# Kernel tuning notes

Hardware: AMD Instinct MI355X
Metric: run time of the kernel (lower is better)

## Reference

```python
import jax, jax.numpy as jnp
import numpy as np

R = 8
INPUT_DIM = 2048
OUTPUT_DIM = 2048
SCALING = 16.0 / R  # lora_alpha / r
TEMPERATURE = 1.0
LN_EPS = 1e-5


def setup_inputs() -> dict:
    key = jax.random.key(0)
    ks = jax.random.split(key, 6)
    bs, seq, ctr_out, ctr_final = 8, 2048, 32, 4
    x = jax.random.normal(ks[0], (bs, seq, INPUT_DIM), dtype=jnp.float32)
    ctr = jax.random.normal(ks[1], (bs, ctr_out), dtype=jnp.float32)
    W1 = jax.random.normal(ks[2], (60, ctr_out), dtype=jnp.float32) * (1.0 / np.sqrt(ctr_out))
    b1 = jnp.zeros((60,), jnp.float32)
    W2 = jax.random.normal(ks[3], (ctr_final, 60), dtype=jnp.float32) * (1.0 / np.sqrt(60))
    b2 = jnp.zeros((ctr_final,), jnp.float32)
    Wa = jax.random.normal(ks[4], (INPUT_DIM * R, ctr_final), dtype=jnp.float32) * 0.02
    Wb = jax.random.normal(ks[5], (R * OUTPUT_DIM, ctr_final), dtype=jnp.float32) * 0.02
    return {
        'x': x, 'ctr_hidden_states': ctr,
        'ln_gamma': jnp.ones((ctr_out,), jnp.float32),
        'ln_beta': jnp.zeros((ctr_out,), jnp.float32),
        'W1': W1, 'b1': b1, 'W2': W2, 'b2': b2, 'Wa': Wa, 'Wb': Wb,
    }


def reference(x, ctr_hidden_states, ln_gamma, ln_beta, W1, b1, W2, b2, Wa, Wb):
    bs = x.shape[0]
    # gating MLP (default which_in_gate branch): LN -> Linear -> ReLU -> Linear
    mu = jnp.mean(ctr_hidden_states, axis=-1, keepdims=True)
    var = jnp.mean(jnp.square(ctr_hidden_states - mu), axis=-1, keepdims=True)
    z = (ctr_hidden_states - mu) * jax.lax.rsqrt(var + LN_EPS) * ln_gamma + ln_beta
    h = jax.nn.relu(z @ W1.T + b1)                 # [bs, 60]
    gate = h @ W2.T + b2                           # [bs, ctr_final_dim]
    # soft routing with softmax
    gate = jax.nn.softmax(gate / TEMPERATURE, axis=-1)
    # per-sample low-rank adapters
    A = (gate @ Wa.T).reshape(bs, R, INPUT_DIM)    # [bs, r, d_in]
    B = (gate @ Wb.T).reshape(bs, R, OUTPUT_DIM)   # [bs, r, d_out]
    # out = (x @ A^T) @ B * scaling
    xa = jnp.einsum('bsd,brd->bsr', x, A)          # [bs, seq, r]
    out = jnp.einsum('bsr,bro->bso', xa, B) * SCALING
    return out
```

## Files before the change

### kernel.cpp

```cpp
#include <hip/hip_runtime.h>
#include <math.h>


#define BS 8
#define SEQ 2048
#define DIM 2048
#define RR 8
#define SCALING 2.0f

typedef float vf4 __attribute__((ext_vector_type(4)));

__global__ void gate_ab_kernel(const float* __restrict__ ctr,
                               const float* __restrict__ gamma,
                               const float* __restrict__ beta,
                               const float* __restrict__ W1,
                               const float* __restrict__ b1,
                               const float* __restrict__ W2,
                               const float* __restrict__ b2,
                               const float* __restrict__ Wa,
                               const float* __restrict__ Wb,
                               float* __restrict__ A,
                               float* __restrict__ B) {
    __shared__ float z_s[BS][32];
    __shared__ float h_s[BS][60];
    __shared__ float logit_s[BS][4];
    __shared__ float gate_s[BS][4];
    const int tid = threadIdx.x;

    {
        const int b = tid >> 5, i = tid & 31;
        float v = ctr[b * 32 + i];
        float s = v;
        #pragma unroll
        for (int m = 16; m; m >>= 1) s += __shfl_xor(s, m, 64);
        const float mu = s * (1.0f / 32.0f);
        const float d = v - mu;
        float sq = d * d;
        #pragma unroll
        for (int m = 16; m; m >>= 1) sq += __shfl_xor(sq, m, 64);
        const float var = sq * (1.0f / 32.0f);
        z_s[b][i] = d * rsqrtf(var + 1e-5f) * gamma[i] + beta[i];
    }
    __syncthreads();

    for (int idx = tid; idx < BS * 60; idx += 256) {
        const int b = idx / 60, j = idx % 60;
        float acc = b1[j];
        #pragma unroll
        for (int k = 0; k < 32; ++k) acc += z_s[b][k] * W1[j * 32 + k];
        h_s[b][j] = fmaxf(acc, 0.0f);
    }
    __syncthreads();

    if (tid < 32) {
        const int b = tid >> 2, c = tid & 3;
        float acc = b2[c];
        for (int k = 0; k < 60; ++k) acc += h_s[b][k] * W2[c * 60 + k];
        logit_s[b][c] = acc;
    }
    __syncthreads();

    if (tid < 8) {
        float m = logit_s[tid][0];
        #pragma unroll
        for (int c = 1; c < 4; ++c) m = fmaxf(m, logit_s[tid][c]);
        float e[4], s = 0.0f;
        #pragma unroll
        for (int c = 0; c < 4; ++c) { e[c] = expf(logit_s[tid][c] - m); s += e[c]; }
        const float inv = 1.0f / s;
        #pragma unroll
        for (int c = 0; c < 4; ++c) gate_s[tid][c] = e[c] * inv;
    }
    __syncthreads();

    const vf4* __restrict__ Wa4 = (const vf4*)Wa;
    const vf4* __restrict__ Wb4 = (const vf4*)Wb;
    const int total = BS * RR * DIM;
    for (int idx = blockIdx.x * 256 + tid; idx < total; idx += gridDim.x * 256) {
        const int b = idx >> 14, rd = idx & 16383;
        const vf4 g = *(const vf4*)gate_s[b];
        const vf4 wa = Wa4[rd];
        A[idx] = g.x * wa.x + g.y * wa.y + g.z * wa.z + g.w * wa.w;
        const vf4 wb = Wb4[rd];
        B[idx] = SCALING * (g.x * wb.x + g.y * wb.y + g.z * wb.z + g.w * wb.w);
    }
}

__global__ void __launch_bounds__(256, 4)
xa_kernel(const float* __restrict__ x, const float* __restrict__ A,
          float* __restrict__ xa) {
    const int b    = blockIdx.x >> 7;
    const int tile = blockIdx.x & 127;
    const int wave = threadIdx.x >> 6, lane = threadIdx.x & 63;
    const int row0 = tile * 16 + wave * 4;

    const float* __restrict__ xr = x + ((size_t)(b * SEQ + row0)) * DIM;
    const float* __restrict__ Ab = A + b * (RR * DIM);

    float acc[4][8];
    #pragma unroll
    for (int i = 0; i < 4; ++i)
        #pragma unroll
        for (int r = 0; r < 8; ++r) acc[i][r] = 0.0f;

    vf4 xcur[4], xnxt[4];
    {
        const int d0 = lane * 4;
        #pragma unroll
        for (int i = 0; i < 4; ++i)
            xcur[i] = *(const vf4*)&xr[(size_t)i * DIM + d0];
    }
    #pragma unroll
    for (int j = 0; j < 8; ++j) {
        const int d = j * 256 + lane * 4;
        if (j < 7) {
            #pragma unroll
            for (int i = 0; i < 4; ++i)
                xnxt[i] = *(const vf4*)&xr[(size_t)i * DIM + d + 256];
        }
        vf4 a4[8];
        #pragma unroll
        for (int r = 0; r < 8; ++r) a4[r] = *(const vf4*)&Ab[r * DIM + d];
        #pragma unroll
        for (int i = 0; i < 4; ++i) {
            #pragma unroll
            for (int r = 0; r < 8; ++r)
                acc[i][r] += xcur[i].x * a4[r].x + xcur[i].y * a4[r].y +
                             xcur[i].z * a4[r].z + xcur[i].w * a4[r].w;
        }
        #pragma unroll
        for (int i = 0; i < 4; ++i) xcur[i] = xnxt[i];
    }

    float xv[4][8];
    #pragma unroll
    for (int i = 0; i < 4; ++i) {
        #pragma unroll
        for (int r = 0; r < 8; ++r) {
            float v = acc[i][r];
            #pragma unroll
            for (int off = 32; off; off >>= 1) v += __shfl_xor(v, off, 64);
            xv[i][r] = v;
        }
    }

    if (lane < 32) {
        float v = 0.0f;
        #pragma unroll
        for (int i = 0; i < 4; ++i)
            #pragma unroll
            for (int r = 0; r < 8; ++r)
                if (lane == i * 8 + r) v = xv[i][r];
        xa[((size_t)(b * SEQ + row0)) * RR + lane] = v;
    }
}

__global__ void __launch_bounds__(256, 4)
out_kernel(const float* __restrict__ xa, const float* __restrict__ B,
           float* __restrict__ out) {
    const int b    = blockIdx.x >> 7;
    const int tile = blockIdx.x & 127;
    const int wave = threadIdx.x >> 6, lane = threadIdx.x & 63;
    const int row0 = tile * 16 + wave * 4;

    const float* __restrict__ Bb = B + b * (RR * DIM);
    float* __restrict__ ob = out + ((size_t)(b * SEQ + row0)) * DIM;

    float xv[4][8];
    #pragma unroll
    for (int i = 0; i < 4; ++i) {
        const vf4 lo = *(const vf4*)&xa[((size_t)(b * SEQ + row0 + i)) * RR];
        const vf4 hi = *(const vf4*)&xa[((size_t)(b * SEQ + row0 + i)) * RR + 4];
        xv[i][0] = lo.x; xv[i][1] = lo.y; xv[i][2] = lo.z; xv[i][3] = lo.w;
        xv[i][4] = hi.x; xv[i][5] = hi.y; xv[i][6] = hi.z; xv[i][7] = hi.w;
    }

    #pragma unroll
    for (int j = 0; j < 8; ++j) {
        const int o = j * 256 + lane * 4;
        vf4 b4[8];
        #pragma unroll
        for (int r = 0; r < 8; ++r) b4[r] = *(const vf4*)&Bb[r * DIM + o];
        #pragma unroll
        for (int i = 0; i < 4; ++i) {
            vf4 v = {0.0f, 0.0f, 0.0f, 0.0f};
            #pragma unroll
            for (int r = 0; r < 8; ++r) {
                v.x += xv[i][r] * b4[r].x;
                v.y += xv[i][r] * b4[r].y;
                v.z += xv[i][r] * b4[r].z;
                v.w += xv[i][r] * b4[r].w;
            }
            *(vf4*)&ob[(size_t)i * DIM + o] = v;
        }
    }
}

extern "C" void kernel_launch(void* const* d_in, const int* in_sizes, int n_in,
                              void* d_out, int out_size, void* d_ws, size_t ws_size,
                              hipStream_t stream) {
    const float* x     = (const float*)d_in[0];
    const float* ctr   = (const float*)d_in[1];
    const float* gamma = (const float*)d_in[2];
    const float* beta  = (const float*)d_in[3];
    const float* W1    = (const float*)d_in[4];
    const float* b1    = (const float*)d_in[5];
    const float* W2    = (const float*)d_in[6];
    const float* b2    = (const float*)d_in[7];
    const float* Wa    = (const float*)d_in[8];
    const float* Wb    = (const float*)d_in[9];

    float* ws = (float*)d_ws;
    float* A  = ws;
    float* B  = ws + 131072;
    float* xa = ws + 262144;
    float* out = (float*)d_out;

    gate_ab_kernel<<<128, 256, 0, stream>>>(ctr, gamma, beta, W1, b1, W2, b2,
                                            Wa, Wb, A, B);
    xa_kernel<<<BS * SEQ / 16, 256, 0, stream>>>(x, A, xa);
    out_kernel<<<BS * SEQ / 16, 256, 0, stream>>>(xa, B, out);
}
```

Measured before the change: 279.1 us.

## Shrink xa tile to two rows per wave and retile out kernel by columns

xa_kernel now handles 2 rows per wave instead of 4, with the launch grid doubled and the occupancy hint raised to 6. The explicit x prefetch double-buffer is dropped to cut register pressure. out_kernel is retiled so each thread keeps a fixed 8-column slice of B in registers and loops over 16 rows, loading B once instead of per row group. The cost is more blocks that each re-read A in xa_kernel, and less explicit latency hiding for x loads.

```diff
diff --git a/kernel.cpp b/kernel.cpp
--- a/kernel.cpp
+++ b/kernel.cpp
@@ -86,55 +86,43 @@
     }
 }
 
-__global__ void __launch_bounds__(256, 4)
+__global__ void __launch_bounds__(256, 6)
 xa_kernel(const float* __restrict__ x, const float* __restrict__ A,
           float* __restrict__ xa) {
-    const int b    = blockIdx.x >> 7;
-    const int tile = blockIdx.x & 127;
+    const int b    = blockIdx.x >> 8;
+    const int tile = blockIdx.x & 255;
     const int wave = threadIdx.x >> 6, lane = threadIdx.x & 63;
-    const int row0 = tile * 16 + wave * 4;
+    const int row0 = tile * 8 + wave * 2;
 
     const float* __restrict__ xr = x + ((size_t)(b * SEQ + row0)) * DIM;
     const float* __restrict__ Ab = A + b * (RR * DIM);
 
-    float acc[4][8];
-    #pragma unroll
-    for (int i = 0; i < 4; ++i)
+    float acc[2][8];
+    #pragma unroll
+    for (int i = 0; i < 2; ++i)
         #pragma unroll
         for (int r = 0; r < 8; ++r) acc[i][r] = 0.0f;
 
-    vf4 xcur[4], xnxt[4];
-    {
-        const int d0 = lane * 4;
-        #pragma unroll
-        for (int i = 0; i < 4; ++i)
-            xcur[i] = *(const vf4*)&xr[(size_t)i * DIM + d0];
-    }
     #pragma unroll
     for (int j = 0; j < 8; ++j) {
         const int d = j * 256 + lane * 4;
-        if (j < 7) {
-            #pragma unroll
-            for (int i = 0; i < 4; ++i)
-                xnxt[i] = *(const vf4*)&xr[(size_t)i * DIM + d + 256];
-        }
+        vf4 xv0 = *(const vf4*)&xr[d];
+        vf4 xv1 = *(const vf4*)&xr[DIM + d];
         vf4 a4[8];
         #pragma unroll
         for (int r = 0; r < 8; ++r) a4[r] = *(const vf4*)&Ab[r * DIM + d];
         #pragma unroll
-        for (int i = 0; i < 4; ++i) {
-            #pragma unroll
-            for (int r = 0; r < 8; ++r)
-                acc[i][r] += xcur[i].x * a4[r].x + xcur[i].y * a4[r].y +
-                             xcur[i].z * a4[r].z + xcur[i].w * a4[r].w;
-        }
-        #pragma unroll
-        for (int i = 0; i < 4; ++i) xcur[i] = xnxt[i];
-    }
-
-    float xv[4][8];
-    #pragma unroll
-    for (int i = 0; i < 4; ++i) {
+        for (int r = 0; r < 8; ++r) {
+            acc[0][r] += xv0.x * a4[r].x + xv0.y * a4[r].y +
+                         xv0.z * a4[r].z + xv0.w * a4[r].w;
+            acc[1][r] += xv1.x * a4[r].x + xv1.y * a4[r].y +
+                         xv1.z * a4[r].z + xv1.w * a4[r].w;
+        }
+    }
+
+    float xv[2][8];
+    #pragma unroll
+    for (int i = 0; i < 2; ++i) {
         #pragma unroll
         for (int r = 0; r < 8; ++r) {
             float v = acc[i][r];
@@ -144,10 +132,10 @@
         }
     }
 
-    if (lane < 32) {
+    if (lane < 16) {
         float v = 0.0f;
         #pragma unroll
-        for (int i = 0; i < 4; ++i)
+        for (int i = 0; i < 2; ++i)
             #pragma unroll
             for (int r = 0; r < 8; ++r)
                 if (lane == i * 8 + r) v = xv[i][r];
@@ -161,38 +149,45 @@
     const int b    = blockIdx.x >> 7;
     const int tile = blockIdx.x & 127;
     const int wave = threadIdx.x >> 6, lane = threadIdx.x & 63;
-    const int row0 = tile * 16 + wave * 4;
+    const int row0 = tile * 16;
+    const int col0 = wave * 512 + lane * 4;
 
     const float* __restrict__ Bb = B + b * (RR * DIM);
-    float* __restrict__ ob = out + ((size_t)(b * SEQ + row0)) * DIM;
-
-    float xv[4][8];
-    #pragma unroll
-    for (int i = 0; i < 4; ++i) {
-        const vf4 lo = *(const vf4*)&xa[((size_t)(b * SEQ + row0 + i)) * RR];
-        const vf4 hi = *(const vf4*)&xa[((size_t)(b * SEQ + row0 + i)) * RR + 4];
-        xv[i][0] = lo.x; xv[i][1] = lo.y; xv[i][2] = lo.z; xv[i][3] = lo.w;
-        xv[i][4] = hi.x; xv[i][5] = hi.y; xv[i][6] = hi.z; xv[i][7] = hi.w;
-    }
-
-    #pragma unroll
-    for (int j = 0; j < 8; ++j) {
-        const int o = j * 256 + lane * 4;
-        vf4 b4[8];
-        #pragma unroll
-        for (int r = 0; r < 8; ++r) b4[r] = *(const vf4*)&Bb[r * DIM + o];
-        #pragma unroll
-        for (int i = 0; i < 4; ++i) {
-            vf4 v = {0.0f, 0.0f, 0.0f, 0.0f};
-            #pragma unroll
-            for (int r = 0; r < 8; ++r) {
-                v.x += xv[i][r] * b4[r].x;
-                v.y += xv[i][r] * b4[r].y;
-                v.z += xv[i][r] * b4[r].z;
-                v.w += xv[i][r] * b4[r].w;
-            }
-            *(vf4*)&ob[(size_t)i * DIM + o] = v;
-        }
+
+    vf4 b0[8], b1[8];
+    #pragma unroll
+    for (int r = 0; r < 8; ++r) {
+        b0[r] = *(const vf4*)&Bb[r * DIM + col0];
+        b1[r] = *(const vf4*)&Bb[r * DIM + col0 + 256];
+    }
+
+    const float* __restrict__ xab = xa + ((size_t)(b * SEQ + row0)) * RR;
+    float* __restrict__ ob = out + ((size_t)(b * SEQ + row0)) * DIM + col0;
+
+    #pragma unroll 2
+    for (int i = 0; i < 16; ++i) {
+        const vf4 xlo = *(const vf4*)&xab[i * RR];
+        const vf4 xhi = *(const vf4*)&xab[i * RR + 4];
+        vf4 o0 = {0.0f, 0.0f, 0.0f, 0.0f};
+        vf4 o1 = {0.0f, 0.0f, 0.0f, 0.0f};
+        #pragma unroll
+        for (int r = 0; r < 4; ++r) {
+            const float f = xlo[r];
+            o0.x += f * b0[r].x; o0.y += f * b0[r].y;
+            o0.z += f * b0[r].z; o0.w += f * b0[r].w;
+            o1.x += f * b1[r].x; o1.y += f * b1[r].y;
+            o1.z += f * b1[r].z; o1.w += f * b1[r].w;
+        }
+        #pragma unroll
+        for (int r = 0; r < 4; ++r) {
+            const float f = xhi[r];
+            o0.x += f * b0[r + 4].x; o0.y += f * b0[r + 4].y;
+            o0.z += f * b0[r + 4].z; o0.w += f * b0[r + 4].w;
+            o1.x += f * b1[r + 4].x; o1.y += f * b1[r + 4].y;
+            o1.z += f * b1[r + 4].z; o1.w += f * b1[r + 4].w;
+        }
+        *(vf4*)&ob[(size_t)i * DIM] = o0;
+        *(vf4*)&ob[(size_t)i * DIM + 256] = o1;
     }
 }
 
@@ -218,6 +213,6 @@
 
     gate_ab_kernel<<<128, 256, 0, stream>>>(ctr, gamma, beta, W1, b1, W2, b2,
                                             Wa, Wb, A, B);
-    xa_kernel<<<BS * SEQ / 16, 256, 0, stream>>>(x, A, xa);
+    xa_kernel<<<BS * SEQ / 8, 256, 0, stream>>>(x, A, xa);
     out_kernel<<<BS * SEQ / 16, 256, 0, stream>>>(xa, B, out);
 }
```

Measured after the change: 280.0 us. Within noise of the previous version (+0.3%).
